# Optimization experiments

Hardware: AMD Instinct MI355X
Metric: run time of the kernel (lower is better)

## Reference

```python
import jax, jax.numpy as jnp
import numpy as np

B, C, H, W = 4, 192, 64, 64
D_STATE, D_CONV, EXPAND = 16, 4, 2
DIN = EXPAND * C            # 384
DT_RANK = (C + 15) // 16    # 12
EPS = 1e-5


def _silu(v):
    return v * jax.nn.sigmoid(v)


def _snake(x2d):
    # x2d: [B, H, W, D]; reverse every odd row (boustrophedon / snake scan).
    # This op is its own inverse.
    odd = (jnp.arange(x2d.shape[1]) % 2 == 1)[None, :, None, None]
    return jnp.where(odd, jnp.flip(x2d, axis=2), x2d)


def setup_inputs() -> dict:
    key = jax.random.key(0)
    ks = jax.random.split(key, 12)
    s = lambda k, shape, sc: jax.random.normal(k, shape, dtype=jnp.float32) * sc
    inp = {
        "x": jax.random.normal(ks[0], (B, C, H, W), dtype=jnp.float32),
        "gn_gamma": jnp.ones((C,), jnp.float32),
        "gn_beta": jnp.zeros((C,), jnp.float32),
        "in_proj_w": s(ks[1], (2 * DIN, C), 0.05),
        "conv1d_w": s(ks[2], (DIN, D_CONV), 0.2),
        "conv1d_b": jnp.zeros((DIN,), jnp.float32),
        "x_proj_w": s(ks[3], (DT_RANK + 2 * D_STATE, DIN), 0.05),
        "dt_proj_w": s(ks[4], (DIN, DT_RANK), 0.1),
        "dt_proj_b": s(ks[5], (DIN,), 0.1),
        "A_log": jnp.log(jnp.broadcast_to(jnp.arange(1, D_STATE + 1, dtype=jnp.float32), (DIN, D_STATE))),
        "Dskip": jnp.ones((DIN,), jnp.float32),
        "le_w": s(ks[6], (DIN, 1, 3, 3), 0.1),      # depthwise 3x3 local enhancement
        "out_proj_w": s(ks[7], (C, DIN), 0.05),
        "proj_out_w": s(ks[8], (C, C), 0.05),        # 1x1 conv, no bias
    }
    return inp


def reference(x, gn_gamma, gn_beta, in_proj_w, conv1d_w, conv1d_b,
              x_proj_w, dt_proj_w, dt_proj_b, A_log, Dskip, le_w,
              out_proj_w, proj_out_w):
    b, c, h, w = x.shape
    L = h * w
    din = DIN

    # GroupNorm(1, C): normalize over (C, H, W) per sample
    mu = jnp.mean(x, axis=(1, 2, 3), keepdims=True)
    var = jnp.var(x, axis=(1, 2, 3), keepdims=True)
    xn = (x - mu) * jax.lax.rsqrt(var + EPS)
    xn = xn * gn_gamma[None, :, None, None] + gn_beta[None, :, None, None]

    xs = xn.reshape(b, c, L).transpose(0, 2, 1)            # [B, L, C]

    # input projection -> (u, z)
    xz = jnp.einsum('blc,dc->bld', xs, in_proj_w)          # [B, L, 2*din]
    u, z = jnp.split(xz, 2, axis=-1)

    # snake scan ordering on u
    u = _snake(u.reshape(b, h, w, din)).reshape(b, L, din)

    # causal depthwise conv1d along sequence + SiLU
    u_t = u.transpose(0, 2, 1)                              # [B, din, L]
    u_c = jax.lax.conv_general_dilated(
        u_t, conv1d_w[:, None, :], (1,), [(D_CONV - 1, 0)],
        feature_group_count=din)
    u_c = _silu(u_c + conv1d_b[None, :, None]).transpose(0, 2, 1)  # [B, L, din]

    # input-dependent SSM parameters
    dbl = jnp.einsum('bld,ed->ble', u_c, x_proj_w)          # [B, L, dt_rank+2N]
    dt, Bm, Cm = jnp.split(dbl, [DT_RANK, DT_RANK + D_STATE], axis=-1)
    delta = jax.nn.softplus(jnp.einsum('blr,dr->bld', dt, dt_proj_w) + dt_proj_b)
    A = -jnp.exp(A_log)                                     # [din, N]

    # selective scan over L steps, carry state [B, din, N]
    def step(hc, inp):
        d_t, B_t, C_t, u_t_ = inp                           # [B,din],[B,N],[B,N],[B,din]
        dA = jnp.exp(d_t[..., None] * A)                    # [B, din, N]
        hc = dA * hc + (d_t * u_t_)[..., None] * B_t[:, None, :]
        y_t = jnp.einsum('bdn,bn->bd', hc, C_t)
        return hc, y_t

    h0 = jnp.zeros((b, din, D_STATE), delta.dtype)
    xs_scan = (delta.transpose(1, 0, 2), Bm.transpose(1, 0, 2),
               Cm.transpose(1, 0, 2), u_c.transpose(1, 0, 2))
    _, ys = jax.lax.scan(step, h0, xs_scan)                 # ys: [L, B, din]
    y = ys.transpose(1, 0, 2) + u_c * Dskip                 # [B, L, din]

    # undo snake ordering (involution), then gate with z (raster order)
    y = _snake(y.reshape(b, h, w, din)).reshape(b, L, din)
    y = y * _silu(z)

    # local enhancement: depthwise 3x3 conv residual on the 2D map
    y2d = y.reshape(b, h, w, din).transpose(0, 3, 1, 2)     # [B, din, H, W]
    y_le = jax.lax.conv_general_dilated(
        y2d, le_w, (1, 1), [(1, 1), (1, 1)], feature_group_count=din)
    y = y + y_le.transpose(0, 2, 3, 1).reshape(b, L, din)

    # output projection back to C, reshape, then 1x1 conv
    out_seq = jnp.einsum('bld,cd->blc', y, out_proj_w)      # [B, L, C]
    out = out_seq.transpose(0, 2, 1).reshape(b, c, h, w)
    out = jnp.einsum('bchw,oc->bohw', out, proj_out_w)
    return out
```

## Files before the change

kernel.cpp:

```cpp
#include <hip/hip_runtime.h>
#include <cstddef>

constexpr int CB  = 4;
constexpr int CC  = 192;
constexpr int CH  = 64;
constexpr int CW  = 64;
constexpr int CL  = CH * CW;
constexpr int DIN = 384;
constexpr int NST = 16;
constexpr int DTR = 12;

constexpr int NCHUNK = 64;
constexpr int NELEM  = CB * DIN * NST;

constexpr int WS_PART  = 0;
constexpr int WS_STAT  = 512;
constexpr int WS_BFIN  = 1024;
constexpr int WS_BFOUT = WS_BFIN + 73728;
constexpr int WS_BFPO  = WS_BFOUT + 36864;
constexpr int WS_BFXF  = WS_BFPO + 18432;
constexpr int WS_LWT   = WS_BFXF + 86016;
constexpr int WS_BIG   = WS_LWT + 3456;
constexpr size_t NBL   = (size_t)CB * CL;
constexpr size_t BIGSZ = NBL * DIN;

using half8 = __attribute__((ext_vector_type(8))) _Float16;
using half4 = __attribute__((ext_vector_type(4))) _Float16;
using f32x4 = __attribute__((ext_vector_type(4))) float;

__device__ __forceinline__ float sigm(float v) { return 1.f / (1.f + __expf(-v)); }
__device__ __forceinline__ float silu_f(float v) { return v * sigm(v); }
__device__ __forceinline__ float softplus_f(float v) { return v > 20.f ? v : log1pf(__expf(v)); }
template <int PAT>
__device__ __forceinline__ float quadswz(float v) {
  return __int_as_float(__builtin_amdgcn_ds_swizzle(__float_as_int(v), PAT));
}

__device__ __forceinline__ size_t afrag_idx(int m, int k, int KS) {
  int m16 = m >> 4, r16 = m & 15;
  int ks = k >> 5, kg = (k & 31) >> 3, j = k & 7;
  return (((size_t)(m16 * KS + ks)) << 9) + (size_t)(((kg << 4) + r16) << 3) + j;
}

__global__ __launch_bounds__(256) void gn_partial(const float* __restrict__ x,
                                                  float* __restrict__ part) {
  int b = blockIdx.x >> 6;
  int chunk = blockIdx.x & 63;
  const float* px = x + (size_t)b * CC * CL + (size_t)chunk * 12288;
  float s = 0.f, s2 = 0.f;
  for (int i = threadIdx.x; i < 12288 / 4; i += 256) {
    float4 v = ((const float4*)px)[i];
    s  += v.x + v.y + v.z + v.w;
    s2 += v.x * v.x + v.y * v.y + v.z * v.z + v.w * v.w;
  }
  __shared__ float ls[4], ls2[4];
  for (int off = 32; off; off >>= 1) { s += __shfl_down(s, off); s2 += __shfl_down(s2, off); }
  int wid = threadIdx.x >> 6, lane = threadIdx.x & 63;
  if (lane == 0) { ls[wid] = s; ls2[wid] = s2; }
  __syncthreads();
  if (threadIdx.x == 0) {
    float t = 0.f, t2 = 0.f;
    for (int i = 0; i < 4; i++) { t += ls[i]; t2 += ls2[i]; }
    part[blockIdx.x * 2] = t;
    part[blockIdx.x * 2 + 1] = t2;
  }
}

__global__ __launch_bounds__(256) void gn_final(const float* __restrict__ part,
                                                float* __restrict__ stat) {
  int b = threadIdx.x >> 6;
  int i = threadIdx.x & 63;
  float s = part[(b * 64 + i) * 2];
  float s2 = part[(b * 64 + i) * 2 + 1];
  for (int off = 32; off; off >>= 1) { s += __shfl_down(s, off); s2 += __shfl_down(s2, off); }
  if (i == 0) {
    float n = (float)(CC * CL);
    float mu = s / n;
    float var = s2 / n - mu * mu;
    stat[b * 2] = mu;
    stat[b * 2 + 1] = rsqrtf(var + 1e-5f);
  }
}

__device__ __forceinline__ void pack_frag(_Float16* dst, int idx, int KS,
                                          const float* __restrict__ W, int KDIM) {
  int j = idx & 7, lane = (idx >> 3) & 63, colq = (idx >> 9) & 3, rest = idx >> 11;
  int ks = rest % KS, nt = rest / KS;
  int col = nt * 64 + colq * 16 + (lane & 15);
  int k = ks * 32 + ((lane >> 4) << 3) + j;
  dst[idx] = (_Float16)W[(size_t)col * KDIM + k];
}

__device__ __forceinline__ void pack_xf(_Float16* dst, int idx,
                                        const float* __restrict__ xw,
                                        const float* __restrict__ dtw) {
  int j = idx & 7, lane = (idx >> 3) & 63, colq = (idx >> 9) & 3, rest = idx >> 11;
  int ks = rest % 12, nt = rest / 12;
  int col = nt * 64 + colq * 16 + (lane & 15);
  int k = ks * 32 + ((lane >> 4) << 3) + j;
  float v = 0.f;
  if (col < 384) {
#pragma unroll
    for (int r = 0; r < 12; r++)
      v += xw[r * 384 + k] * dtw[col * 12 + r];
  } else if (col < 416) {
    v = xw[(col - 384 + 12) * 384 + k];
  }
  dst[idx] = (_Float16)v;
}

__global__ __launch_bounds__(256) void transpose_all(
    const float* __restrict__ in_proj_w, const float* __restrict__ x_proj_w,
    const float* __restrict__ dt_proj_w, const float* __restrict__ out_proj_w,
    const float* __restrict__ proj_out_w, const float* __restrict__ le_w,
    float* __restrict__ ws) {
  int idx = blockIdx.x * 256 + threadIdx.x;
  if (idx < 147456) {
    pack_frag((_Float16*)(ws + WS_BFIN), idx, 6, in_proj_w, 192);
    return;
  }
  idx -= 147456;
  if (idx < 73728) {
    pack_frag((_Float16*)(ws + WS_BFOUT), idx, 12, out_proj_w, 384);
    return;
  }
  idx -= 73728;
  if (idx < 36864) {
    pack_frag((_Float16*)(ws + WS_BFPO), idx, 6, proj_out_w, 192);
    return;
  }
  idx -= 36864;
  if (idx < 172032) {
    pack_xf((_Float16*)(ws + WS_BFXF), idx, x_proj_w, dt_proj_w);
    return;
  }
  idx -= 172032;
  if (idx < 3456) {
    int t9 = idx / 384, d = idx % 384;
    ws[WS_LWT + idx] = le_w[d * 9 + t9];
  }
}

__global__ __launch_bounds__(256) void gemm_inproj_mfma(
    const float* __restrict__ x, const _Float16* __restrict__ Bf,
    const float* __restrict__ stat, const float* __restrict__ gamma,
    const float* __restrict__ beta, float* __restrict__ u, float* __restrict__ z) {
  int mt = blockIdx.x & 255, nt = blockIdx.x >> 8;
  int m0 = mt * 64;
  int b = m0 >> 12, l0 = m0 & 4095;
  float mu = stat[b * 2], rs = stat[b * 2 + 1];
  __shared__ __align__(16) _Float16 Ah[64][200];
  int tid = threadIdx.x;
  int row = tid & 63, cq = tid >> 6;
#pragma unroll
  for (int i = 0; i < 12; i++) {
    int c0 = cq * 4 + i * 16;
    half4 h;
#pragma unroll
    for (int cc = 0; cc < 4; cc++) {
      int c = c0 + cc;
      float g = gamma[c] * rs;
      float bt = beta[c] - mu * g;
      float xv = x[((size_t)(b * 192 + c) << 12) + l0 + row];
      h[cc] = (_Float16)(xv * g + bt);
    }
    *(half4*)&Ah[row][c0] = h;
  }
  __syncthreads();
  int w = tid >> 6, lane = tid & 63;
  int wm = (w >> 1) * 32, wcol = w & 1;
  int r16 = lane & 15, kg = lane >> 4;
  f32x4 acc[2][2] = {};
#pragma unroll
  for (int ks = 0; ks < 6; ks++) {
    half8 a0 = *(const half8*)&Ah[wm + r16][ks * 32 + kg * 8];
    half8 a1 = *(const half8*)&Ah[wm + 16 + r16][ks * 32 + kg * 8];
    half8 b0 = *(const half8*)&Bf[(((size_t)(nt * 6 + ks) * 4 + wcol * 2 + 0) << 9) + lane * 8];
    half8 b1 = *(const half8*)&Bf[(((size_t)(nt * 6 + ks) * 4 + wcol * 2 + 1) << 9) + lane * 8];
    acc[0][0] = __builtin_amdgcn_mfma_f32_16x16x32_f16(a0, b0, acc[0][0], 0, 0, 0);
    acc[0][1] = __builtin_amdgcn_mfma_f32_16x16x32_f16(a0, b1, acc[0][1], 0, 0, 0);
    acc[1][0] = __builtin_amdgcn_mfma_f32_16x16x32_f16(a1, b0, acc[1][0], 0, 0, 0);
    acc[1][1] = __builtin_amdgcn_mfma_f32_16x16x32_f16(a1, b1, acc[1][1], 0, 0, 0);
  }
  int hrow = l0 >> 6;
  bool odd = hrow & 1;
#pragma unroll
  for (int mi = 0; mi < 2; mi++)
#pragma unroll
    for (int ni = 0; ni < 2; ni++)
#pragma unroll
      for (int r = 0; r < 4; r++) {
        int wloc = wm + mi * 16 + kg * 4 + r;
        int d = nt * 64 + wcol * 32 + ni * 16 + r16;
        float val = acc[mi][ni][r];
        if (d < DIN) {
          int ls = odd ? (hrow << 6) + 63 - wloc : l0 + wloc;
          u[((size_t)(b << 12) + ls) * DIN + d] = val;
        } else {
          z[((size_t)(b << 12) + l0 + wloc) * DIN + (d - DIN)] = val;
        }
      }
}

__global__ __launch_bounds__(256) void xfull_direct(
    const _Float16* __restrict__ Af, const _Float16* __restrict__ Bf,
    const float* __restrict__ dt_bias, float* __restrict__ delta,
    float* __restrict__ Bmb, float* __restrict__ Cmb) {
  int mt = blockIdx.x & 255, nt = blockIdx.x >> 8;
  int m0 = mt * 64;
  int tid = threadIdx.x;
  int w = tid >> 6, lane = tid & 63;
  int wm = (w >> 1) * 32, wcol = w & 1;
  int r16 = lane & 15, kg = lane >> 4;
  int m16a = (m0 + wm) >> 4;
  f32x4 acc[2][2] = {};
#pragma unroll
  for (int ks = 0; ks < 12; ks++) {
    half8 a0 = *(const half8*)&Af[(((size_t)(m16a * 12 + ks)) << 9) + lane * 8];
    half8 a1 = *(const half8*)&Af[(((size_t)((m16a + 1) * 12 + ks)) << 9) + lane * 8];
    half8 b0 = *(const half8*)&Bf[(((size_t)(nt * 12 + ks) * 4 + wcol * 2 + 0) << 9) + lane * 8];
    half8 b1 = *(const half8*)&Bf[(((size_t)(nt * 12 + ks) * 4 + wcol * 2 + 1) << 9) + lane * 8];
    acc[0][0] = __builtin_amdgcn_mfma_f32_16x16x32_f16(a0, b0, acc[0][0], 0, 0, 0);
    acc[0][1] = __builtin_amdgcn_mfma_f32_16x16x32_f16(a0, b1, acc[0][1], 0, 0, 0);
    acc[1][0] = __builtin_amdgcn_mfma_f32_16x16x32_f16(a1, b0, acc[1][0], 0, 0, 0);
    acc[1][1] = __builtin_amdgcn_mfma_f32_16x16x32_f16(a1, b1, acc[1][1], 0, 0, 0);
  }
#pragma unroll
  for (int mi = 0; mi < 2; mi++)
#pragma unroll
    for (int ni = 0; ni < 2; ni++)
#pragma unroll
      for (int r = 0; r < 4; r++) {
        size_t m = m0 + wm + mi * 16 + kg * 4 + r;
        int gc = nt * 64 + wcol * 32 + ni * 16 + r16;
        float val = acc[mi][ni][r];
        if (gc < 384)
          delta[m * DIN + gc] = softplus_f(val + dt_bias[gc]);
        else if (gc < 400)
          Bmb[m * 16 + (gc - 384)] = val;
        else if (gc < 416)
          Cmb[m * 16 + (gc - 400)] = val;
      }
}

__global__ __launch_bounds__(256) void gemm_out_direct(
    const _Float16* __restrict__ Af, const _Float16* __restrict__ Bf,
    _Float16* __restrict__ outh) {
  int mt = blockIdx.x & 255, nt = blockIdx.x >> 8;
  int m0 = mt * 64;
  int tid = threadIdx.x;
  int w = tid >> 6, lane = tid & 63;
  int wm = (w >> 1) * 32, wcol = w & 1;
  int r16 = lane & 15, kg = lane >> 4;
  int m16a = (m0 + wm) >> 4;
  f32x4 acc[2][2] = {};
#pragma unroll
  for (int ks = 0; ks < 12; ks++) {
    half8 a0 = *(const half8*)&Af[(((size_t)(m16a * 12 + ks)) << 9) + lane * 8];
    half8 a1 = *(const half8*)&Af[(((size_t)((m16a + 1) * 12 + ks)) << 9) + lane * 8];
    half8 b0 = *(const half8*)&Bf[(((size_t)(nt * 12 + ks) * 4 + wcol * 2 + 0) << 9) + lane * 8];
    half8 b1 = *(const half8*)&Bf[(((size_t)(nt * 12 + ks) * 4 + wcol * 2 + 1) << 9) + lane * 8];
    acc[0][0] = __builtin_amdgcn_mfma_f32_16x16x32_f16(a0, b0, acc[0][0], 0, 0, 0);
    acc[0][1] = __builtin_amdgcn_mfma_f32_16x16x32_f16(a0, b1, acc[0][1], 0, 0, 0);
    acc[1][0] = __builtin_amdgcn_mfma_f32_16x16x32_f16(a1, b0, acc[1][0], 0, 0, 0);
    acc[1][1] = __builtin_amdgcn_mfma_f32_16x16x32_f16(a1, b1, acc[1][1], 0, 0, 0);
  }
  __shared__ float Cs[64][69];
#pragma unroll
  for (int mi = 0; mi < 2; mi++)
#pragma unroll
    for (int ni = 0; ni < 2; ni++)
#pragma unroll
      for (int r = 0; r < 4; r++)
        Cs[wm + mi * 16 + kg * 4 + r][wcol * 32 + ni * 16 + r16] = acc[mi][ni][r];
  __syncthreads();
  int pair = tid >> 5, l32 = tid & 31;
  int mi2 = pair >> 1, ksl = pair & 1;
#pragma unroll
  for (int it = 0; it < 2; it++) {
    int lane2 = l32 + it * 32;
    int r16b = lane2 & 15, kgb = lane2 >> 4;
    int rowl = mi2 * 16 + r16b;
    int coll = ksl * 32 + kgb * 8;
    half8 h;
#pragma unroll
    for (int jj = 0; jj < 8; jj++) h[jj] = (_Float16)Cs[rowl][coll + jj];
    size_t m16o = (size_t)((m0 >> 4) + mi2);
    int kso = nt * 2 + ksl;
    *(half8*)&outh[((m16o * 6 + kso) << 9) + lane2 * 8] = h;
  }
}

__global__ __launch_bounds__(256) void gemm_po_direct(
    const _Float16* __restrict__ Af, const _Float16* __restrict__ Bf,
    float* __restrict__ C) {
  int mt = blockIdx.x & 255, nt = blockIdx.x >> 8;
  int m0 = mt * 64, n0 = nt * 64;
  int tid = threadIdx.x;
  int w = tid >> 6, lane = tid & 63;
  int wm = (w >> 1) * 32, wcol = w & 1;
  int r16 = lane & 15, kg = lane >> 4;
  int m16a = (m0 + wm) >> 4;
  f32x4 acc[2][2] = {};
#pragma unroll
  for (int ks = 0; ks < 6; ks++) {
    half8 a0 = *(const half8*)&Af[(((size_t)(m16a * 6 + ks)) << 9) + lane * 8];
    half8 a1 = *(const half8*)&Af[(((size_t)((m16a + 1) * 6 + ks)) << 9) + lane * 8];
    half8 b0 = *(const half8*)&Bf[(((size_t)(nt * 6 + ks) * 4 + wcol * 2 + 0) << 9) + lane * 8];
    half8 b1 = *(const half8*)&Bf[(((size_t)(nt * 6 + ks) * 4 + wcol * 2 + 1) << 9) + lane * 8];
    acc[0][0] = __builtin_amdgcn_mfma_f32_16x16x32_f16(a0, b0, acc[0][0], 0, 0, 0);
    acc[0][1] = __builtin_amdgcn_mfma_f32_16x16x32_f16(a0, b1, acc[0][1], 0, 0, 0);
    acc[1][0] = __builtin_amdgcn_mfma_f32_16x16x32_f16(a1, b0, acc[1][0], 0, 0, 0);
    acc[1][1] = __builtin_amdgcn_mfma_f32_16x16x32_f16(a1, b1, acc[1][1], 0, 0, 0);
  }
  __shared__ float Cs[64][69];
#pragma unroll
  for (int mi = 0; mi < 2; mi++)
#pragma unroll
    for (int ni = 0; ni < 2; ni++)
#pragma unroll
      for (int r = 0; r < 4; r++)
        Cs[wcol * 32 + ni * 16 + r16][wm + mi * 16 + kg * 4 + r] = acc[mi][ni][r];
  __syncthreads();
  int b = m0 >> 12, l0 = m0 & 4095;
  int li = tid & 63;
#pragma unroll
  for (int rr = 0; rr < 16; rr++) {
    int o = rr * 4 + (tid >> 6);
    C[(size_t)(b * CC + n0 + o) * CL + l0 + li] = Cs[o][li];
  }
}

__global__ __launch_bounds__(256) void conv_silu_tiled(
    const float* __restrict__ u, const float* __restrict__ cw,
    const float* __restrict__ cb, float* __restrict__ uc,
    _Float16* __restrict__ uc_h) {
  int bid = blockIdx.x;
  int dg = bid % 6;
  int lt = (bid / 6) % 64;
  int b  = bid / (6 * 64);
  int d0 = dg * 64;
  int l0 = lt * 64;
  __shared__ float S[67][68];
  int t = threadIdx.x;
  for (int idx = t; idx < 67 * 16; idx += 256) {
    int row = idx >> 4, c4i = idx & 15;
    int l = l0 + row - 3;
    float4 v = make_float4(0.f, 0.f, 0.f, 0.f);
    if (l >= 0)
      v = *(const float4*)&u[((size_t)((b << 12) + l)) * DIN + d0 + c4i * 4];
    *(float4*)&S[row][c4i * 4] = v;
  }
  __syncthreads();
  int c4 = t & 15, j0 = (t >> 4) << 2;
  int dd = d0 + c4 * 4;
  float4 cwv[4];
#pragma unroll
  for (int i = 0; i < 4; i++) cwv[i] = *(const float4*)&cw[(dd + i) * 4];
  float4 bias = *(const float4*)&cb[dd];
  float4 win[7];
#pragma unroll
  for (int k = 0; k < 7; k++) win[k] = *(float4*)&S[j0 + k][c4 * 4];
#pragma unroll
  for (int j = 0; j < 4; j++) {
    float4 acc = bias;
#pragma unroll
    for (int k = 0; k < 4; k++) {
      float4 v = win[j + k];
      acc.x = fmaf(v.x, ((const float*)&cwv[0])[k], acc.x);
      acc.y = fmaf(v.y, ((const float*)&cwv[1])[k], acc.y);
      acc.z = fmaf(v.z, ((const float*)&cwv[2])[k], acc.z);
      acc.w = fmaf(v.w, ((const float*)&cwv[3])[k], acc.w);
    }
    acc.x = silu_f(acc.x);
    acc.y = silu_f(acc.y);
    acc.z = silu_f(acc.z);
    acc.w = silu_f(acc.w);
    int l = l0 + j0 + j;
    int m = (b << 12) + l;
    *(float4*)&uc[(size_t)m * DIN + dd] = acc;
    half4 h;
    h[0] = (_Float16)acc.x; h[1] = (_Float16)acc.y;
    h[2] = (_Float16)acc.z; h[3] = (_Float16)acc.w;
    *(half4*)&uc_h[afrag_idx(m, dd, 12)] = h;
  }
}

__global__ __launch_bounds__(256) void scan_partial(
    const float* __restrict__ delta, const float* __restrict__ uc,
    const float* __restrict__ Bmb, const float* __restrict__ A_log,
    float* __restrict__ hend, float* __restrict__ Pbuf) {
  int bid = blockIdx.x;
  int chunk = bid & 63, bg = bid >> 6;
  int b = bg / 6, g = bg % 6;
  int t = threadIdx.x;
  int dloc = t >> 2, q = t & 3;
  int d = g * 64 + dloc;
  __shared__ float sD[64][64], sU[64][64], sB[64][16];
  size_t baseBL = ((size_t)b << 12) + chunk * 64;
  {
    int row = t >> 2, cg = (t & 3) * 16;
    const float* dp = &delta[(baseBL + row) * DIN + g * 64 + cg];
    const float* up = &uc[(baseBL + row) * DIN + g * 64 + cg];
#pragma unroll
    for (int c = 0; c < 4; c++) {
      *(float4*)&sD[row][cg + 4 * c] = *(const float4*)&dp[4 * c];
      *(float4*)&sU[row][cg + 4 * c] = *(const float4*)&up[4 * c];
    }
    *(float4*)&sB[row][q * 4] = *(const float4*)&Bmb[(baseBL + row) * 16 + q * 4];
  }
  __syncthreads();
  float4 av = *(const float4*)&A_log[d * 16 + 4 * q];
  float a0 = -__expf(av.x), a1 = -__expf(av.y), a2 = -__expf(av.z), a3 = -__expf(av.w);
  float h0 = 0.f, h1 = 0.f, h2 = 0.f, h3 = 0.f, sdel = 0.f;
#pragma unroll 8
  for (int ll = 0; ll < 64; ll++) {
    float dv = sD[ll][dloc];
    float uv = sU[ll][dloc];
    float4 Bv = *(const float4*)&sB[ll][q * 4];
    float duv = dv * uv;
    h0 = fmaf(__expf(dv * a0), h0, duv * Bv.x);
    h1 = fmaf(__expf(dv * a1), h1, duv * Bv.y);
    h2 = fmaf(__expf(dv * a2), h2, duv * Bv.z);
    h3 = fmaf(__expf(dv * a3), h3, duv * Bv.w);
    sdel += dv;
  }
  size_t e = ((size_t)(b * DIN + d)) * 16 + 4 * q;
  float4 hv; hv.x = h0; hv.y = h1; hv.z = h2; hv.w = h3;
  *(float4*)&hend[(size_t)chunk * NELEM + e] = hv;
  float4 pv;
  pv.x = __expf(a0 * sdel); pv.y = __expf(a1 * sdel);
  pv.z = __expf(a2 * sdel); pv.w = __expf(a3 * sdel);
  *(float4*)&Pbuf[(size_t)chunk * NELEM + e] = pv;
}

__global__ __launch_bounds__(256) void scan_combine(
    const float* __restrict__ hend, const float* __restrict__ Pbuf,
    float* __restrict__ hin) {
  int e = blockIdx.x * 256 + threadIdx.x;
  float h = 0.f;
  float Pc = Pbuf[e], Hc = hend[e];
#pragma unroll 8
  for (int c = 0; c < NCHUNK; c++) {
    float Pn = 0.f, Hn = 0.f;
    if (c < NCHUNK - 1) {
      Pn = Pbuf[(size_t)(c + 1) * NELEM + e];
      Hn = hend[(size_t)(c + 1) * NELEM + e];
    }
    hin[(size_t)c * NELEM + e] = h;
    h = fmaf(Pc, h, Hc);
    Pc = Pn; Hc = Hn;
  }
}

__global__ __launch_bounds__(256) void scan_final(
    const float* __restrict__ delta, const float* __restrict__ uc,
    const float* __restrict__ Bmb, const float* __restrict__ Cmb,
    const float* __restrict__ A_log, const float* __restrict__ Dskip,
    const float* __restrict__ z, const float* __restrict__ hin,
    float* __restrict__ yr) {
  int bid = blockIdx.x;
  int chunk = bid & 63, bg = bid >> 6;
  int b = bg / 6, g = bg % 6;
  int t = threadIdx.x;
  int dloc = t >> 2, q = t & 3;
  int d = g * 64 + dloc;
  __shared__ float sD[64][64], sU[64][64], sB[64][16], sC[64][16];
  size_t baseBL = ((size_t)b << 12) + chunk * 64;
  {
    int row = t >> 2, cg = (t & 3) * 16;
    const float* dp = &delta[(baseBL + row) * DIN + g * 64 + cg];
    const float* up = &uc[(baseBL + row) * DIN + g * 64 + cg];
#pragma unroll
    for (int c = 0; c < 4; c++) {
      *(float4*)&sD[row][cg + 4 * c] = *(const float4*)&dp[4 * c];
      *(float4*)&sU[row][cg + 4 * c] = *(const float4*)&up[4 * c];
    }
    *(float4*)&sB[row][q * 4] = *(const float4*)&Bmb[(baseBL + row) * 16 + q * 4];
    *(float4*)&sC[row][q * 4] = *(const float4*)&Cmb[(baseBL + row) * 16 + q * 4];
  }
  __syncthreads();
  float4 av = *(const float4*)&A_log[d * 16 + 4 * q];
  float a0 = -__expf(av.x), a1 = -__expf(av.y), a2 = -__expf(av.z), a3 = -__expf(av.w);
  size_t e = ((size_t)(b * DIN + d)) * 16 + 4 * q;
  float4 hv = *(const float4*)&hin[(size_t)chunk * NELEM + e];
  float h0 = hv.x, h1 = hv.y, h2 = hv.z, h3 = hv.w;
  float yk[16];
#pragma unroll
  for (int ll = 0; ll < 64; ll++) {
    float dv = sD[ll][dloc];
    float uv = sU[ll][dloc];
    float4 Bv = *(const float4*)&sB[ll][q * 4];
    float4 Cv = *(const float4*)&sC[ll][q * 4];
    float duv = dv * uv;
    h0 = fmaf(__expf(dv * a0), h0, duv * Bv.x);
    h1 = fmaf(__expf(dv * a1), h1, duv * Bv.y);
    h2 = fmaf(__expf(dv * a2), h2, duv * Bv.z);
    h3 = fmaf(__expf(dv * a3), h3, duv * Bv.w);
    float yp = h0 * Cv.x + h1 * Cv.y + h2 * Cv.z + h3 * Cv.w;
    yp += quadswz<0x041F>(yp);
    yp += quadswz<0x081F>(yp);
    if ((ll & 3) == q) yk[ll >> 2] = yp;
  }
  float dsk = Dskip[d];
  bool odd = chunk & 1;
#pragma unroll
  for (int i = 0; i < 16; i++) {
    int ll = 4 * i + q;
    int wr = odd ? 63 - ll : ll;
    size_t ro = baseBL + wr;
    float uvll = sU[ll][dloc];
    float zv = z[ro * DIN + d];
    yr[ro * DIN + d] = (yk[i] + uvll * dsk) * silu_f(zv);
  }
}

__global__ __launch_bounds__(256) void le_conv_tiled(
    const float* __restrict__ yr, const float* __restrict__ lwT,
    _Float16* __restrict__ y2h) {
  int bid = blockIdx.x;
  int dg = bid % 24;
  int ht = (bid / 24) % 16;
  int b  = bid / (24 * 16);
  int d0 = dg * 16;
  int h0 = ht * 4;
  __shared__ float S[6][66][24];
  int t = threadIdx.x;
  int dq = t & 3, w = t >> 2;
#pragma unroll
  for (int r = 0; r < 6; r++) {
    int hh = h0 - 1 + r;
    float4 v = make_float4(0.f, 0.f, 0.f, 0.f);
    if (hh >= 0 && hh < 64)
      v = *(const float4*)&yr[((size_t)((b << 12) + (hh << 6) + w)) * DIN + d0 + dq * 4];
    *(float4*)&S[r][w + 1][dq * 4] = v;
    if (w == 0)  *(float4*)&S[r][0][dq * 4]  = make_float4(0.f, 0.f, 0.f, 0.f);
    if (w == 63) *(float4*)&S[r][65][dq * 4] = make_float4(0.f, 0.f, 0.f, 0.f);
  }
  __syncthreads();
  float4 wv[9];
#pragma unroll
  for (int i = 0; i < 9; i++)
    wv[i] = *(const float4*)&lwT[i * DIN + d0 + dq * 4];
#pragma unroll
  for (int hr = 0; hr < 4; hr++) {
    float4 acc = *(float4*)&S[hr + 1][w + 1][dq * 4];
#pragma unroll
    for (int ki = 0; ki < 3; ki++)
#pragma unroll
      for (int kj = 0; kj < 3; kj++) {
        float4 v = *(float4*)&S[hr + ki][w + kj][dq * 4];
        float4 c = wv[ki * 3 + kj];
        acc.x = fmaf(v.x, c.x, acc.x);
        acc.y = fmaf(v.y, c.y, acc.y);
        acc.z = fmaf(v.z, c.z, acc.z);
        acc.w = fmaf(v.w, c.w, acc.w);
      }
    int l = ((h0 + hr) << 6) + w;
    int m = (b << 12) + l;
    half4 h;
    h[0] = (_Float16)acc.x; h[1] = (_Float16)acc.y;
    h[2] = (_Float16)acc.z; h[3] = (_Float16)acc.w;
    *(half4*)&y2h[afrag_idx(m, d0 + dq * 4, 12)] = h;
  }
}

extern "C" void kernel_launch(void* const* d_in, const int* in_sizes, int n_in,
                              void* d_out, int out_size, void* d_ws, size_t ws_size,
                              hipStream_t stream) {
  const float* x          = (const float*)d_in[0];
  const float* gn_gamma   = (const float*)d_in[1];
  const float* gn_beta    = (const float*)d_in[2];
  const float* in_proj_w  = (const float*)d_in[3];
  const float* conv1d_w   = (const float*)d_in[4];
  const float* conv1d_b   = (const float*)d_in[5];
  const float* x_proj_w   = (const float*)d_in[6];
  const float* dt_proj_w  = (const float*)d_in[7];
  const float* dt_proj_b  = (const float*)d_in[8];
  const float* A_log      = (const float*)d_in[9];
  const float* Dskip      = (const float*)d_in[10];
  const float* le_w       = (const float*)d_in[11];
  const float* out_proj_w = (const float*)d_in[12];
  const float* proj_out_w = (const float*)d_in[13];
  float* out = (float*)d_out;

  float* ws      = (float*)d_ws;
  float* part    = ws + WS_PART;
  float* stat    = ws + WS_STAT;
  _Float16* BfIn  = (_Float16*)(ws + WS_BFIN);
  _Float16* BfOut = (_Float16*)(ws + WS_BFOUT);
  _Float16* BfPo  = (_Float16*)(ws + WS_BFPO);
  _Float16* BfXf  = (_Float16*)(ws + WS_BFXF);
  float* lwT    = ws + WS_LWT;
  float* u      = ws + WS_BIG;
  float* zb     = u + BIGSZ;
  float* uc     = zb + BIGSZ;
  float* delta  = uc + BIGSZ;
  float* yr     = delta + BIGSZ;
  float* Bmb    = yr + BIGSZ;
  float* Cmb    = Bmb + NBL * NST;
  _Float16* uc_h = (_Float16*)yr;
  _Float16* y2h  = (_Float16*)delta;
  _Float16* outh = (_Float16*)zb;
  float* hend   = u;
  float* Pbuf   = u + (size_t)NCHUNK * NELEM;
  float* hin    = u + 2 * (size_t)NCHUNK * NELEM;

  gn_partial<<<256, 256, 0, stream>>>(x, part);
  gn_final<<<1, 256, 0, stream>>>(part, stat);
  transpose_all<<<1694, 256, 0, stream>>>(in_proj_w, x_proj_w, dt_proj_w,
                                          out_proj_w, proj_out_w, le_w, ws);
  gemm_inproj_mfma<<<256 * 12, 256, 0, stream>>>(x, BfIn, stat, gn_gamma, gn_beta, u, zb);
  conv_silu_tiled<<<1536, 256, 0, stream>>>(u, conv1d_w, conv1d_b, uc, uc_h);
  xfull_direct<<<256 * 7, 256, 0, stream>>>(uc_h, BfXf, dt_proj_b, delta, Bmb, Cmb);
  scan_partial<<<1536, 256, 0, stream>>>(delta, uc, Bmb, A_log, hend, Pbuf);
  scan_combine<<<96, 256, 0, stream>>>(hend, Pbuf, hin);
  scan_final<<<1536, 256, 0, stream>>>(delta, uc, Bmb, Cmb, A_log, Dskip,
                                       zb, hin, yr);
  le_conv_tiled<<<1536, 256, 0, stream>>>(yr, lwT, y2h);
  gemm_out_direct<<<256 * 3, 256, 0, stream>>>(y2h, BfOut, outh);
  gemm_po_direct<<<256 * 3, 256, 0, stream>>>(outh, BfPo, out);
}
```

Baseline: 261.9 us.

## Fold out_proj and proj_out weights into one GEMM, merge prep kernels, coalesce stores

Precomputes the product of proj_out_w and out_proj_w once per call in a prep kernel, so the last two GEMMs and their half-precision intermediate become a single K=384 GEMM. The groupnorm partial sums and weight packing are merged into that one prep launch, removing a kernel launch. GEMM epilogues in in_proj, xfull and scan_final now stage results in shared memory and write float4-coalesced rows instead of scattered scalar stores. This adds extra syncthreads and LDS traffic, and the fused weight is rounded to fp16 once rather than the intermediate activation, which changes numerics slightly.

```diff
diff --git a/kernel.cpp b/kernel.cpp
--- a/kernel.cpp
+++ b/kernel.cpp
@@ -16,9 +16,8 @@
 constexpr int WS_PART  = 0;
 constexpr int WS_STAT  = 512;
 constexpr int WS_BFIN  = 1024;
-constexpr int WS_BFOUT = WS_BFIN + 73728;
-constexpr int WS_BFPO  = WS_BFOUT + 36864;
-constexpr int WS_BFXF  = WS_BFPO + 18432;
+constexpr int WS_W2F   = WS_BFIN + 73728;
+constexpr int WS_BFXF  = WS_W2F + 36864;
 constexpr int WS_LWT   = WS_BFXF + 86016;
 constexpr int WS_BIG   = WS_LWT + 3456;
 constexpr size_t NBL   = (size_t)CB * CL;
@@ -41,28 +40,119 @@
   int ks = k >> 5, kg = (k & 31) >> 3, j = k & 7;
   return (((size_t)(m16 * KS + ks)) << 9) + (size_t)(((kg << 4) + r16) << 3) + j;
 }
-
-__global__ __launch_bounds__(256) void gn_partial(const float* __restrict__ x,
-                                                  float* __restrict__ part) {
-  int b = blockIdx.x >> 6;
-  int chunk = blockIdx.x & 63;
-  const float* px = x + (size_t)b * CC * CL + (size_t)chunk * 12288;
-  float s = 0.f, s2 = 0.f;
-  for (int i = threadIdx.x; i < 12288 / 4; i += 256) {
-    float4 v = ((const float4*)px)[i];
-    s  += v.x + v.y + v.z + v.w;
-    s2 += v.x * v.x + v.y * v.y + v.z * v.z + v.w * v.w;
-  }
+__device__ __forceinline__ size_t bfrag_idx(int col, int k, int KS) {
+  int nt = col >> 6, colq = (col >> 4) & 3, r16 = col & 15;
+  int ks = k >> 5, kg = (k & 31) >> 3, j = k & 7;
+  return (((size_t)((nt * KS + ks) * 4 + colq)) << 9) + (size_t)(((kg << 4) + r16) << 3) + j;
+}
+
+__device__ __forceinline__ void pack_frag(_Float16* dst, int idx, int KS,
+                                          const float* __restrict__ W, int KDIM) {
+  int j = idx & 7, lane = (idx >> 3) & 63, colq = (idx >> 9) & 3, rest = idx >> 11;
+  int ks = rest % KS, nt = rest / KS;
+  int col = nt * 64 + colq * 16 + (lane & 15);
+  int k = ks * 32 + ((lane >> 4) << 3) + j;
+  dst[idx] = (_Float16)W[(size_t)col * KDIM + k];
+}
+
+__device__ __forceinline__ void pack_xf(_Float16* dst, int idx,
+                                        const float* __restrict__ xw,
+                                        const float* __restrict__ dtw) {
+  int j = idx & 7, lane = (idx >> 3) & 63, colq = (idx >> 9) & 3, rest = idx >> 11;
+  int ks = rest % 12, nt = rest / 12;
+  int col = nt * 64 + colq * 16 + (lane & 15);
+  int k = ks * 32 + ((lane >> 4) << 3) + j;
+  float v = 0.f;
+  if (col < 384) {
+#pragma unroll
+    for (int r = 0; r < 12; r++)
+      v += xw[r * 384 + k] * dtw[col * 12 + r];
+  } else if (col < 416) {
+    v = xw[(col - 384 + 12) * 384 + k];
+  }
+  dst[idx] = (_Float16)v;
+}
+
+__global__ __launch_bounds__(256) void prep_kernel(
+    const float* __restrict__ x, const float* __restrict__ in_proj_w,
+    const float* __restrict__ x_proj_w, const float* __restrict__ dt_proj_w,
+    const float* __restrict__ out_proj_w, const float* __restrict__ proj_out_w,
+    const float* __restrict__ le_w, float* __restrict__ ws) {
+  __shared__ float Ps[16][65];
+  __shared__ float Os[16][65];
   __shared__ float ls[4], ls2[4];
-  for (int off = 32; off; off >>= 1) { s += __shfl_down(s, off); s2 += __shfl_down(s2, off); }
-  int wid = threadIdx.x >> 6, lane = threadIdx.x & 63;
-  if (lane == 0) { ls[wid] = s; ls2[wid] = s2; }
-  __syncthreads();
-  if (threadIdx.x == 0) {
-    float t = 0.f, t2 = 0.f;
-    for (int i = 0; i < 4; i++) { t += ls[i]; t2 += ls2[i]; }
-    part[blockIdx.x * 2] = t;
-    part[blockIdx.x * 2 + 1] = t2;
+  int bid = blockIdx.x;
+  int tid = threadIdx.x;
+  if (bid < 18) {
+    int ct = bid / 6, kt = bid % 6;
+    int co0 = ct * 64, k0 = kt * 64;
+    int tx = tid & 15, ty = tid >> 4;
+    float acc[4][4] = {};
+    for (int c0 = 0; c0 < 192; c0 += 16) {
+      for (int i2 = tid; i2 < 1024; i2 += 256) {
+        int cc = i2 >> 6, e = i2 & 63;
+        Ps[cc][e] = proj_out_w[(size_t)(co0 + e) * 192 + c0 + cc];
+        Os[cc][e] = out_proj_w[(size_t)(c0 + cc) * 384 + k0 + e];
+      }
+      __syncthreads();
+#pragma unroll
+      for (int kk = 0; kk < 16; kk++) {
+        float a[4], b[4];
+#pragma unroll
+        for (int i = 0; i < 4; i++) a[i] = Ps[kk][tx + 16 * i];
+#pragma unroll
+        for (int j = 0; j < 4; j++) b[j] = Os[kk][ty + 16 * j];
+#pragma unroll
+        for (int i = 0; i < 4; i++)
+#pragma unroll
+          for (int j = 0; j < 4; j++) acc[i][j] = fmaf(a[i], b[j], acc[i][j]);
+      }
+      __syncthreads();
+    }
+    _Float16* w2f = (_Float16*)(ws + WS_W2F);
+#pragma unroll
+    for (int i = 0; i < 4; i++)
+#pragma unroll
+      for (int j = 0; j < 4; j++)
+        w2f[bfrag_idx(co0 + tx + 16 * i, k0 + ty + 16 * j, 12)] = (_Float16)acc[i][j];
+    return;
+  }
+  if (bid < 18 + 256) {
+    int gid = bid - 18;
+    int b = gid >> 6, chunk = gid & 63;
+    const float* px = x + (size_t)b * CC * CL + (size_t)chunk * 12288;
+    float s = 0.f, s2 = 0.f;
+    for (int i = tid; i < 12288 / 4; i += 256) {
+      float4 v = ((const float4*)px)[i];
+      s  += v.x + v.y + v.z + v.w;
+      s2 += v.x * v.x + v.y * v.y + v.z * v.z + v.w * v.w;
+    }
+    for (int off = 32; off; off >>= 1) { s += __shfl_down(s, off); s2 += __shfl_down(s2, off); }
+    int wid = tid >> 6, lane = tid & 63;
+    if (lane == 0) { ls[wid] = s; ls2[wid] = s2; }
+    __syncthreads();
+    if (tid == 0) {
+      float t = 0.f, t2 = 0.f;
+      for (int i = 0; i < 4; i++) { t += ls[i]; t2 += ls2[i]; }
+      ws[WS_PART + gid * 2] = t;
+      ws[WS_PART + gid * 2 + 1] = t2;
+    }
+    return;
+  }
+  int idx = (bid - 274) * 256 + tid;
+  if (idx < 147456) {
+    pack_frag((_Float16*)(ws + WS_BFIN), idx, 6, in_proj_w, 192);
+    return;
+  }
+  idx -= 147456;
+  if (idx < 172032) {
+    pack_xf((_Float16*)(ws + WS_BFXF), idx, x_proj_w, dt_proj_w);
+    return;
+  }
+  idx -= 172032;
+  if (idx < 3456) {
+    int t9 = idx / 384, d = idx % 384;
+    ws[WS_LWT + idx] = le_w[d * 9 + t9];
   }
 }
 
@@ -82,65 +172,6 @@
   }
 }
 
-__device__ __forceinline__ void pack_frag(_Float16* dst, int idx, int KS,
-                                          const float* __restrict__ W, int KDIM) {
-  int j = idx & 7, lane = (idx >> 3) & 63, colq = (idx >> 9) & 3, rest = idx >> 11;
-  int ks = rest % KS, nt = rest / KS;
-  int col = nt * 64 + colq * 16 + (lane & 15);
-  int k = ks * 32 + ((lane >> 4) << 3) + j;
-  dst[idx] = (_Float16)W[(size_t)col * KDIM + k];
-}
-
-__device__ __forceinline__ void pack_xf(_Float16* dst, int idx,
-                                        const float* __restrict__ xw,
-                                        const float* __restrict__ dtw) {
-  int j = idx & 7, lane = (idx >> 3) & 63, colq = (idx >> 9) & 3, rest = idx >> 11;
-  int ks = rest % 12, nt = rest / 12;
-  int col = nt * 64 + colq * 16 + (lane & 15);
-  int k = ks * 32 + ((lane >> 4) << 3) + j;
-  float v = 0.f;
-  if (col < 384) {
-#pragma unroll
-    for (int r = 0; r < 12; r++)
-      v += xw[r * 384 + k] * dtw[col * 12 + r];
-  } else if (col < 416) {
-    v = xw[(col - 384 + 12) * 384 + k];
-  }
-  dst[idx] = (_Float16)v;
-}
-
-__global__ __launch_bounds__(256) void transpose_all(
-    const float* __restrict__ in_proj_w, const float* __restrict__ x_proj_w,
-    const float* __restrict__ dt_proj_w, const float* __restrict__ out_proj_w,
-    const float* __restrict__ proj_out_w, const float* __restrict__ le_w,
-    float* __restrict__ ws) {
-  int idx = blockIdx.x * 256 + threadIdx.x;
-  if (idx < 147456) {
-    pack_frag((_Float16*)(ws + WS_BFIN), idx, 6, in_proj_w, 192);
-    return;
-  }
-  idx -= 147456;
-  if (idx < 73728) {
-    pack_frag((_Float16*)(ws + WS_BFOUT), idx, 12, out_proj_w, 384);
-    return;
-  }
-  idx -= 73728;
-  if (idx < 36864) {
-    pack_frag((_Float16*)(ws + WS_BFPO), idx, 6, proj_out_w, 192);
-    return;
-  }
-  idx -= 36864;
-  if (idx < 172032) {
-    pack_xf((_Float16*)(ws + WS_BFXF), idx, x_proj_w, dt_proj_w);
-    return;
-  }
-  idx -= 172032;
-  if (idx < 3456) {
-    int t9 = idx / 384, d = idx % 384;
-    ws[WS_LWT + idx] = le_w[d * 9 + t9];
-  }
-}
-
 __global__ __launch_bounds__(256) void gemm_inproj_mfma(
     const float* __restrict__ x, const _Float16* __restrict__ Bf,
     const float* __restrict__ stat, const float* __restrict__ gamma,
@@ -182,24 +213,31 @@
     acc[1][0] = __builtin_amdgcn_mfma_f32_16x16x32_f16(a1, b0, acc[1][0], 0, 0, 0);
     acc[1][1] = __builtin_amdgcn_mfma_f32_16x16x32_f16(a1, b1, acc[1][1], 0, 0, 0);
   }
+  float* CsF = (float*)&Ah[0][0];
+  __syncthreads();
+#pragma unroll
+  for (int mi = 0; mi < 2; mi++)
+#pragma unroll
+    for (int ni = 0; ni < 2; ni++)
+#pragma unroll
+      for (int r = 0; r < 4; r++)
+        CsF[(wm + mi * 16 + kg * 4 + r) * 68 + wcol * 32 + ni * 16 + r16] = acc[mi][ni][r];
+  __syncthreads();
   int hrow = l0 >> 6;
   bool odd = hrow & 1;
-#pragma unroll
-  for (int mi = 0; mi < 2; mi++)
-#pragma unroll
-    for (int ni = 0; ni < 2; ni++)
-#pragma unroll
-      for (int r = 0; r < 4; r++) {
-        int wloc = wm + mi * 16 + kg * 4 + r;
-        int d = nt * 64 + wcol * 32 + ni * 16 + r16;
-        float val = acc[mi][ni][r];
-        if (d < DIN) {
-          int ls = odd ? (hrow << 6) + 63 - wloc : l0 + wloc;
-          u[((size_t)(b << 12) + ls) * DIN + d] = val;
-        } else {
-          z[((size_t)(b << 12) + l0 + wloc) * DIN + (d - DIN)] = val;
-        }
-      }
+  int srow = tid >> 2, fq = tid & 3;
+  if (nt < 6) {
+    int ls = odd ? (hrow << 6) + 63 - srow : l0 + srow;
+    float* dst = &u[((size_t)(b << 12) + ls) * DIN + nt * 64 + fq * 16];
+#pragma unroll
+    for (int c = 0; c < 4; c++)
+      *(float4*)&dst[c * 4] = *(float4*)&CsF[srow * 68 + fq * 16 + c * 4];
+  } else {
+    float* dst = &z[((size_t)(b << 12) + l0 + srow) * DIN + (nt - 6) * 64 + fq * 16];
+#pragma unroll
+    for (int c = 0; c < 4; c++)
+      *(float4*)&dst[c * 4] = *(float4*)&CsF[srow * 68 + fq * 16 + c * 4];
+  }
 }
 
 __global__ __launch_bounds__(256) void xfull_direct(
@@ -208,6 +246,7 @@
     float* __restrict__ Bmb, float* __restrict__ Cmb) {
   int mt = blockIdx.x & 255, nt = blockIdx.x >> 8;
   int m0 = mt * 64;
+  __shared__ float Cs[64][68];
   int tid = threadIdx.x;
   int w = tid >> 6, lane = tid & 63;
   int wm = (w >> 1) * 32, wcol = w & 1;
@@ -225,73 +264,48 @@
     acc[1][0] = __builtin_amdgcn_mfma_f32_16x16x32_f16(a1, b0, acc[1][0], 0, 0, 0);
     acc[1][1] = __builtin_amdgcn_mfma_f32_16x16x32_f16(a1, b1, acc[1][1], 0, 0, 0);
   }
-#pragma unroll
-  for (int mi = 0; mi < 2; mi++)
-#pragma unroll
-    for (int ni = 0; ni < 2; ni++)
-#pragma unroll
-      for (int r = 0; r < 4; r++) {
-        size_t m = m0 + wm + mi * 16 + kg * 4 + r;
-        int gc = nt * 64 + wcol * 32 + ni * 16 + r16;
-        float val = acc[mi][ni][r];
-        if (gc < 384)
-          delta[m * DIN + gc] = softplus_f(val + dt_bias[gc]);
-        else if (gc < 400)
-          Bmb[m * 16 + (gc - 384)] = val;
-        else if (gc < 416)
-          Cmb[m * 16 + (gc - 400)] = val;
-      }
-}
-
-__global__ __launch_bounds__(256) void gemm_out_direct(
-    const _Float16* __restrict__ Af, const _Float16* __restrict__ Bf,
-    _Float16* __restrict__ outh) {
-  int mt = blockIdx.x & 255, nt = blockIdx.x >> 8;
-  int m0 = mt * 64;
-  int tid = threadIdx.x;
-  int w = tid >> 6, lane = tid & 63;
-  int wm = (w >> 1) * 32, wcol = w & 1;
-  int r16 = lane & 15, kg = lane >> 4;
-  int m16a = (m0 + wm) >> 4;
-  f32x4 acc[2][2] = {};
-#pragma unroll
-  for (int ks = 0; ks < 12; ks++) {
-    half8 a0 = *(const half8*)&Af[(((size_t)(m16a * 12 + ks)) << 9) + lane * 8];
-    half8 a1 = *(const half8*)&Af[(((size_t)((m16a + 1) * 12 + ks)) << 9) + lane * 8];
-    half8 b0 = *(const half8*)&Bf[(((size_t)(nt * 12 + ks) * 4 + wcol * 2 + 0) << 9) + lane * 8];
-    half8 b1 = *(const half8*)&Bf[(((size_t)(nt * 12 + ks) * 4 + wcol * 2 + 1) << 9) + lane * 8];
-    acc[0][0] = __builtin_amdgcn_mfma_f32_16x16x32_f16(a0, b0, acc[0][0], 0, 0, 0);
-    acc[0][1] = __builtin_amdgcn_mfma_f32_16x16x32_f16(a0, b1, acc[0][1], 0, 0, 0);
-    acc[1][0] = __builtin_amdgcn_mfma_f32_16x16x32_f16(a1, b0, acc[1][0], 0, 0, 0);
-    acc[1][1] = __builtin_amdgcn_mfma_f32_16x16x32_f16(a1, b1, acc[1][1], 0, 0, 0);
-  }
-  __shared__ float Cs[64][69];
-#pragma unroll
-  for (int mi = 0; mi < 2; mi++)
-#pragma unroll
-    for (int ni = 0; ni < 2; ni++)
-#pragma unroll
-      for (int r = 0; r < 4; r++)
-        Cs[wm + mi * 16 + kg * 4 + r][wcol * 32 + ni * 16 + r16] = acc[mi][ni][r];
-  __syncthreads();
-  int pair = tid >> 5, l32 = tid & 31;
-  int mi2 = pair >> 1, ksl = pair & 1;
-#pragma unroll
-  for (int it = 0; it < 2; it++) {
-    int lane2 = l32 + it * 32;
-    int r16b = lane2 & 15, kgb = lane2 >> 4;
-    int rowl = mi2 * 16 + r16b;
-    int coll = ksl * 32 + kgb * 8;
-    half8 h;
-#pragma unroll
-    for (int jj = 0; jj < 8; jj++) h[jj] = (_Float16)Cs[rowl][coll + jj];
-    size_t m16o = (size_t)((m0 >> 4) + mi2);
-    int kso = nt * 2 + ksl;
-    *(half8*)&outh[((m16o * 6 + kso) << 9) + lane2 * 8] = h;
-  }
-}
-
-__global__ __launch_bounds__(256) void gemm_po_direct(
+  if (nt < 6) {
+#pragma unroll
+    for (int mi = 0; mi < 2; mi++)
+#pragma unroll
+      for (int ni = 0; ni < 2; ni++)
+#pragma unroll
+        for (int r = 0; r < 4; r++)
+          Cs[wm + mi * 16 + kg * 4 + r][wcol * 32 + ni * 16 + r16] = acc[mi][ni][r];
+    __syncthreads();
+    int srow = tid >> 2, fq = tid & 3;
+    size_t m = m0 + srow;
+    int gc0 = nt * 64 + fq * 16;
+#pragma unroll
+    for (int c = 0; c < 4; c++) {
+      float4 v = *(float4*)&Cs[srow][fq * 16 + c * 4];
+      float4 bsv = *(const float4*)&dt_bias[gc0 + c * 4];
+      float4 o;
+      o.x = softplus_f(v.x + bsv.x);
+      o.y = softplus_f(v.y + bsv.y);
+      o.z = softplus_f(v.z + bsv.z);
+      o.w = softplus_f(v.w + bsv.w);
+      *(float4*)&delta[m * DIN + gc0 + c * 4] = o;
+    }
+  } else {
+#pragma unroll
+    for (int mi = 0; mi < 2; mi++)
+#pragma unroll
+      for (int ni = 0; ni < 2; ni++)
+#pragma unroll
+        for (int r = 0; r < 4; r++) {
+          size_t m = m0 + wm + mi * 16 + kg * 4 + r;
+          int gc = 384 + wcol * 32 + ni * 16 + r16;
+          float val = acc[mi][ni][r];
+          if (gc < 400)
+            Bmb[m * 16 + (gc - 384)] = val;
+          else if (gc < 416)
+            Cmb[m * 16 + (gc - 400)] = val;
+        }
+  }
+}
+
+__global__ __launch_bounds__(256) void gemm_final_direct(
     const _Float16* __restrict__ Af, const _Float16* __restrict__ Bf,
     float* __restrict__ C) {
   int mt = blockIdx.x & 255, nt = blockIdx.x >> 8;
@@ -303,17 +317,17 @@
   int m16a = (m0 + wm) >> 4;
   f32x4 acc[2][2] = {};
 #pragma unroll
-  for (int ks = 0; ks < 6; ks++) {
-    half8 a0 = *(const half8*)&Af[(((size_t)(m16a * 6 + ks)) << 9) + lane * 8];
-    half8 a1 = *(const half8*)&Af[(((size_t)((m16a + 1) * 6 + ks)) << 9) + lane * 8];
-    half8 b0 = *(const half8*)&Bf[(((size_t)(nt * 6 + ks) * 4 + wcol * 2 + 0) << 9) + lane * 8];
-    half8 b1 = *(const half8*)&Bf[(((size_t)(nt * 6 + ks) * 4 + wcol * 2 + 1) << 9) + lane * 8];
+  for (int ks = 0; ks < 12; ks++) {
+    half8 a0 = *(const half8*)&Af[(((size_t)(m16a * 12 + ks)) << 9) + lane * 8];
+    half8 a1 = *(const half8*)&Af[(((size_t)((m16a + 1) * 12 + ks)) << 9) + lane * 8];
+    half8 b0 = *(const half8*)&Bf[(((size_t)(nt * 12 + ks) * 4 + wcol * 2 + 0) << 9) + lane * 8];
+    half8 b1 = *(const half8*)&Bf[(((size_t)(nt * 12 + ks) * 4 + wcol * 2 + 1) << 9) + lane * 8];
     acc[0][0] = __builtin_amdgcn_mfma_f32_16x16x32_f16(a0, b0, acc[0][0], 0, 0, 0);
     acc[0][1] = __builtin_amdgcn_mfma_f32_16x16x32_f16(a0, b1, acc[0][1], 0, 0, 0);
     acc[1][0] = __builtin_amdgcn_mfma_f32_16x16x32_f16(a1, b0, acc[1][0], 0, 0, 0);
     acc[1][1] = __builtin_amdgcn_mfma_f32_16x16x32_f16(a1, b1, acc[1][1], 0, 0, 0);
   }
-  __shared__ float Cs[64][69];
+  __shared__ float Cs[64][68];
 #pragma unroll
   for (int mi = 0; mi < 2; mi++)
 #pragma unroll
@@ -323,12 +337,11 @@
         Cs[wcol * 32 + ni * 16 + r16][wm + mi * 16 + kg * 4 + r] = acc[mi][ni][r];
   __syncthreads();
   int b = m0 >> 12, l0 = m0 & 4095;
-  int li = tid & 63;
-#pragma unroll
-  for (int rr = 0; rr < 16; rr++) {
-    int o = rr * 4 + (tid >> 6);
-    C[(size_t)(b * CC + n0 + o) * CL + l0 + li] = Cs[o][li];
-  }
+  int o = tid >> 2, fq = tid & 3;
+  float* dst = &C[(size_t)(b * CC + n0 + o) * CL + l0 + fq * 16];
+#pragma unroll
+  for (int c = 0; c < 4; c++)
+    *(float4*)&dst[c * 4] = *(float4*)&Cs[o][fq * 16 + c * 4];
 }
 
 __global__ __launch_bounds__(256) void conv_silu_tiled(
@@ -508,10 +521,21 @@
   for (int i = 0; i < 16; i++) {
     int ll = 4 * i + q;
     int wr = odd ? 63 - ll : ll;
-    size_t ro = baseBL + wr;
-    float uvll = sU[ll][dloc];
-    float zv = z[ro * DIN + d];
-    yr[ro * DIN + d] = (yk[i] + uvll * dsk) * silu_f(zv);
+    sD[wr][dloc] = yk[i] + sU[ll][dloc] * dsk;
+  }
+  __syncthreads();
+  int srow = t >> 2, fq = t & 3;
+  size_t ro = baseBL + srow;
+#pragma unroll
+  for (int c = 0; c < 4; c++) {
+    float4 yv = *(float4*)&sD[srow][fq * 16 + c * 4];
+    float4 zv = *(const float4*)&z[ro * DIN + g * 64 + fq * 16 + c * 4];
+    float4 o;
+    o.x = yv.x * silu_f(zv.x);
+    o.y = yv.y * silu_f(zv.y);
+    o.z = yv.z * silu_f(zv.z);
+    o.w = yv.w * silu_f(zv.w);
+    *(float4*)&yr[ro * DIN + g * 64 + fq * 16 + c * 4] = o;
   }
 }
 
@@ -587,10 +611,9 @@
   float* ws      = (float*)d_ws;
   float* part    = ws + WS_PART;
   float* stat    = ws + WS_STAT;
-  _Float16* BfIn  = (_Float16*)(ws + WS_BFIN);
-  _Float16* BfOut = (_Float16*)(ws + WS_BFOUT);
-  _Float16* BfPo  = (_Float16*)(ws + WS_BFPO);
-  _Float16* BfXf  = (_Float16*)(ws + WS_BFXF);
+  _Float16* BfIn = (_Float16*)(ws + WS_BFIN);
+  _Float16* W2f  = (_Float16*)(ws + WS_W2F);
+  _Float16* BfXf = (_Float16*)(ws + WS_BFXF);
   float* lwT    = ws + WS_LWT;
   float* u      = ws + WS_BIG;
   float* zb     = u + BIGSZ;
@@ -601,15 +624,13 @@
   float* Cmb    = Bmb + NBL * NST;
   _Float16* uc_h = (_Float16*)yr;
   _Float16* y2h  = (_Float16*)delta;
-  _Float16* outh = (_Float16*)zb;
   float* hend   = u;
   float* Pbuf   = u + (size_t)NCHUNK * NELEM;
   float* hin    = u + 2 * (size_t)NCHUNK * NELEM;
 
-  gn_partial<<<256, 256, 0, stream>>>(x, part);
+  prep_kernel<<<1536, 256, 0, stream>>>(x, in_proj_w, x_proj_w, dt_proj_w,
+                                        out_proj_w, proj_out_w, le_w, ws);
   gn_final<<<1, 256, 0, stream>>>(part, stat);
-  transpose_all<<<1694, 256, 0, stream>>>(in_proj_w, x_proj_w, dt_proj_w,
-                                          out_proj_w, proj_out_w, le_w, ws);
   gemm_inproj_mfma<<<256 * 12, 256, 0, stream>>>(x, BfIn, stat, gn_gamma, gn_beta, u, zb);
   conv_silu_tiled<<<1536, 256, 0, stream>>>(u, conv1d_w, conv1d_b, uc, uc_h);
   xfull_direct<<<256 * 7, 256, 0, stream>>>(uc_h, BfXf, dt_proj_b, delta, Bmb, Cmb);
@@ -618,6 +639,5 @@
   scan_final<<<1536, 256, 0, stream>>>(delta, uc, Bmb, Cmb, A_log, Dskip,
                                        zb, hin, yr);
   le_conv_tiled<<<1536, 256, 0, stream>>>(yr, lwT, y2h);
-  gemm_out_direct<<<256 * 3, 256, 0, stream>>>(y2h, BfOut, outh);
-  gemm_po_direct<<<256 * 3, 256, 0, stream>>>(outh, BfPo, out);
-}
+  gemm_final_direct<<<256 * 3, 256, 0, stream>>>(y2h, W2f, out);
+}
```

Measured after the change: 283.3 us. 8.2% more time.
